# Kernel tuning notes

Measured on AMD Instinct MI355X. Metric: run time of the kernel, lower is better.

The kernel has to match this reference:

```python
import jax, jax.numpy as jnp
import numpy as np

LATENT = 128
HIDDEN = 512
N_STEPS = 50
BATCH = 8192


def _linear_init(k, fan_in, fan_out):
    kw, kb = jax.random.split(k)
    lim = 1.0 / np.sqrt(fan_in)
    W = jax.random.uniform(kw, (fan_in, fan_out), minval=-lim, maxval=lim, dtype=jnp.float32)
    b = jax.random.uniform(kb, (fan_out,), minval=-lim, maxval=lim, dtype=jnp.float32)
    return W, b


def setup_inputs() -> dict:
    key = jax.random.key(0)
    ks = jax.random.split(key, 6)
    in_dim = 2 * LATENT + 2  # x + condition + t_emb + target_emb
    W1, b1 = _linear_init(ks[0], in_dim, HIDDEN)
    W2, b2 = _linear_init(ks[1], HIDDEN, HIDDEN)
    W3, b3 = _linear_init(ks[2], HIDDEN, HIDDEN)
    W4, b4 = _linear_init(ks[3], HIDDEN, LATENT)
    condition = jax.random.normal(ks[4], (BATCH, LATENT), dtype=jnp.float32)
    x_init = jax.random.normal(ks[5], (BATCH, LATENT), dtype=jnp.float32)
    return dict(condition=condition, x_init=x_init,
                W1=W1, b1=b1, W2=W2, b2=b2, W3=W3, b3=b3, W4=W4, b4=b4,
                target_survival=1)


def reference(condition, x_init, W1, b1, W2, b2, W3, b3, W4, b4, target_survival):
    n_steps = N_STEPS
    betas = jnp.linspace(1e-4, 0.02, n_steps).astype(x_init.dtype)
    alphas = 1.0 - betas
    alphas_cumprod = jnp.cumprod(alphas)
    batch = condition.shape[0]
    # target = zeros if target_survival else ones (static python scalar)
    target = jnp.full((batch, 1), 0.0 if target_survival else 1.0, dtype=x_init.dtype)
    noise_key = jax.random.key(42)

    def step(x, t):
        t_emb = jnp.full((batch, 1), 1.0, x.dtype) * (t.astype(x.dtype) / n_steps)
        inp = jnp.concatenate([x, condition, t_emb, target], axis=-1)  # [B, 2L+2]
        h = jax.nn.gelu(inp @ W1 + b1, approximate=False)
        h = jax.nn.gelu(h @ W2 + b2, approximate=False)
        h = jax.nn.gelu(h @ W3 + b3, approximate=False)
        noise_pred = h @ W4 + b4  # [B, L]
        noise = jax.random.normal(jax.random.fold_in(noise_key, t), x.shape, x.dtype)
        noise = jnp.where(t > 0, noise, jnp.zeros_like(noise))  # no noise at t=0
        beta_t = betas[t]
        x = (x - beta_t / jnp.sqrt(1.0 - alphas_cumprod[t]) * noise_pred) / jnp.sqrt(alphas[t])
        x = x + jnp.sqrt(beta_t) * noise
        return x, None

    ts = jnp.arange(n_steps - 1, -1, -1)  # reversed(range(n_steps))
    x_final, _ = jax.lax.scan(step, x_init, ts)
    return x_final
```

## Files before the change

kernel.cpp:

```cpp
#include <hip/hip_runtime.h>
#include <stdint.h>
#include <stddef.h>


typedef __bf16 bf16;
typedef __bf16 bf16x4 __attribute__((ext_vector_type(4)));
typedef __bf16 bf16x8 __attribute__((ext_vector_type(8)));
typedef float  floatx4 __attribute__((ext_vector_type(4)));

#define NSTEPS    50
#define WG_ROWS   32
#define XB_STRIDE 136
#define H_STRIDE  520

__device__ __forceinline__ uint32_t rotl32(uint32_t x, int r) {
  return __builtin_amdgcn_alignbit(x, x, 32u - (uint32_t)r);
}

__device__ __forceinline__ void threefry2x32(uint32_t k0, uint32_t k1,
                                             uint32_t x0, uint32_t x1,
                                             uint32_t& o0, uint32_t& o1) {
  uint32_t k2 = k0 ^ k1 ^ 0x1BD11BDAu;
  x0 += k0; x1 += k1;
#define TF_R(R) { x0 += x1; x1 = rotl32(x1, R); x1 ^= x0; }
  TF_R(13) TF_R(15) TF_R(26) TF_R(6)
  x0 += k1; x1 += k2 + 1u;
  TF_R(17) TF_R(29) TF_R(16) TF_R(24)
  x0 += k2; x1 += k0 + 2u;
  TF_R(13) TF_R(15) TF_R(26) TF_R(6)
  x0 += k0; x1 += k1 + 3u;
  TF_R(17) TF_R(29) TF_R(16) TF_R(24)
  x0 += k1; x1 += k2 + 4u;
  TF_R(13) TF_R(15) TF_R(26) TF_R(6)
  x0 += k2; x1 += k0 + 5u;
#undef TF_R
  o0 = x0; o1 = x1;
}

__device__ __forceinline__ float erfinv_xla(float x) {
  float w = -0.6931471805599453f * __builtin_amdgcn_logf(fmaf(-x, x, 1.0f));
  float p;
  if (w < 5.0f) {
    w -= 2.5f;
    p = 2.81022636e-08f;
    p = fmaf(p, w, 3.43273939e-07f);
    p = fmaf(p, w, -3.5233877e-06f);
    p = fmaf(p, w, -4.39150654e-06f);
    p = fmaf(p, w, 0.00021858087f);
    p = fmaf(p, w, -0.00125372503f);
    p = fmaf(p, w, -0.00417768164f);
    p = fmaf(p, w, 0.246640727f);
    p = fmaf(p, w, 1.50140941f);
  } else {
    w = __builtin_amdgcn_sqrtf(w) - 3.0f;
    p = -0.000200214257f;
    p = fmaf(p, w, 0.000100950558f);
    p = fmaf(p, w, 0.00134934322f);
    p = fmaf(p, w, -0.00367342844f);
    p = fmaf(p, w, 0.00573950773f);
    p = fmaf(p, w, -0.0076224613f);
    p = fmaf(p, w, 0.00943887047f);
    p = fmaf(p, w, 1.00167406f);
    p = fmaf(p, w, 2.83297682f);
  }
  return p * x;
}

__device__ __forceinline__ float gelu_fast(float x) {
  float z  = x * 0.7071067811865475f;
  float az = fabsf(z);
  float t  = __builtin_amdgcn_rcpf(fmaf(0.3275911f, az, 1.0f));
  float p  = fmaf(1.061405429f, t, -1.453152027f);
  p = fmaf(p, t, 1.421413741f);
  p = fmaf(p, t, -0.284496736f);
  p = fmaf(p, t, 0.254829592f);
  p *= t;
  float e  = __builtin_amdgcn_exp2f(az * az * -1.4426950408889634f);
  float er = fmaf(-p, e, 1.0f);
  er = copysignf(er, z);
  return 0.5f * x * (1.0f + er);
}

template<int KSTEPS, int BSTRIDE, int UNROLL>
__device__ __forceinline__ void gemm2t(const bf16* __restrict__ h_lds,
                                       const bf16* __restrict__ A_pk,
                                       int lane, floatx4 (&acc)[2][2]) {
  const int nrow = lane & 15, q = lane >> 4;
  const bf16* b0 = h_lds + nrow * BSTRIDE + q * 8;
  const bf16* a0 = A_pk + lane * 8;
#pragma unroll UNROLL
  for (int ks = 0; ks < KSTEPS; ++ks) {
    bf16x8 bf0 = *(const bf16x8*)(b0 + ks * 32);
    bf16x8 bf1 = *(const bf16x8*)(b0 + 16 * BSTRIDE + ks * 32);
    bf16x8 aA  = *(const bf16x8*)(a0 + ks * 512);
    bf16x8 aB  = *(const bf16x8*)(a0 + (KSTEPS + ks) * 512);
    acc[0][0] = __builtin_amdgcn_mfma_f32_16x16x32_bf16(aA, bf0, acc[0][0], 0, 0, 0);
    acc[0][1] = __builtin_amdgcn_mfma_f32_16x16x32_bf16(aA, bf1, acc[0][1], 0, 0, 0);
    acc[1][0] = __builtin_amdgcn_mfma_f32_16x16x32_bf16(aB, bf0, acc[1][0], 0, 0, 0);
    acc[1][1] = __builtin_amdgcn_mfma_f32_16x16x32_bf16(aB, bf1, acc[1][1], 0, 0, 0);
  }
}

template<int KSTEPS, int BSTRIDE>
__device__ __forceinline__ void gemm1t(const bf16* __restrict__ h_lds,
                                       const bf16* __restrict__ A_pk,
                                       int lane, floatx4& acc) {
  const int nrow = lane & 15, q = lane >> 4;
  const bf16* b0 = h_lds + nrow * BSTRIDE + q * 8;
  const bf16* a0 = A_pk + lane * 8;
#pragma unroll 4
  for (int ks = 0; ks < KSTEPS; ++ks) {
    bf16x8 bfr = *(const bf16x8*)(b0 + ks * 32);
    bf16x8 af  = *(const bf16x8*)(a0 + ks * 512);
    acc = __builtin_amdgcn_mfma_f32_16x16x32_bf16(af, bfr, acc, 0, 0, 0);
  }
}

__global__ void diff_prep(const float* __restrict__ W1, const float* __restrict__ b1,
                          const float* __restrict__ W2, const float* __restrict__ W3,
                          const float* __restrict__ W4, const int* __restrict__ tsurv,
                          bf16* __restrict__ w1p, bf16* __restrict__ w1cp,
                          bf16* __restrict__ w2p, bf16* __restrict__ w3p,
                          bf16* __restrict__ w4p,
                          float* __restrict__ eb1, uint32_t* __restrict__ fk,
                          float* __restrict__ cst) {
  const int tid = blockIdx.x * blockDim.x + threadIdx.x;
  const int nth = gridDim.x * blockDim.x;
  for (int i = tid; i < 512 * 128; i += nth) {
    int j = i & 7, lane = (i >> 3) & 63, ks = (i >> 9) & 3, ntg = i >> 11;
    int n = ntg * 16 + (lane & 15);
    int k = ks * 32 + (lane >> 4) * 8 + j;
    w1p[i]  = (bf16)W1[k * 512 + n];
    w1cp[i] = (bf16)W1[(128 + k) * 512 + n];
  }
  for (int i = tid; i < 512 * 512; i += nth) {
    int j = i & 7, lane = (i >> 3) & 63, ks = (i >> 9) & 15, ntg = i >> 13;
    int n = ntg * 16 + (lane & 15);
    int k = ks * 32 + (lane >> 4) * 8 + j;
    w2p[i] = (bf16)W2[k * 512 + n];
    w3p[i] = (bf16)W3[k * 512 + n];
  }
  for (int i = tid; i < 128 * 512; i += nth) {
    int j = i & 7, lane = (i >> 3) & 63, ks = (i >> 9) & 15, ntg = i >> 13;
    int n = ntg * 16 + (lane & 15);
    int k = ks * 32 + (lane >> 4) * 8 + j;
    w4p[i] = (bf16)W4[k * 128 + n];
  }
  const float tgt = (tsurv[0] != 0) ? 0.0f : 1.0f;
  for (int i = tid; i < NSTEPS * 512; i += nth) {
    int t = i >> 9, n = i & 511;
    eb1[i] = b1[n] + ((float)t / 50.0f) * W1[256 * 512 + n] + tgt * W1[257 * 512 + n];
  }
  if (tid == 0) {
    float ac = 1.0f;
    for (int t = 0; t < NSTEPS; ++t) {
      float beta  = 1e-4f + (0.02f - 1e-4f) * ((float)t / 49.0f);
      float alpha = 1.0f - beta;
      ac *= alpha;
      cst[t]            = beta / sqrtf(1.0f - ac);
      cst[NSTEPS + t]   = 1.0f / sqrtf(alpha);
      cst[2*NSTEPS + t] = sqrtf(beta);
      uint32_t o0, o1;
      threefry2x32(0u, 42u, 0u, (uint32_t)t, o0, o1);
      fk[t] = o0; fk[NSTEPS + t] = o1;
    }
  }
}

__global__ __launch_bounds__(1024, 4) void diff_main(
    const float* __restrict__ cond, const float* __restrict__ xinit,
    const bf16* __restrict__ w1p, const bf16* __restrict__ w1cp,
    const bf16* __restrict__ w2p, const bf16* __restrict__ w3p,
    const bf16* __restrict__ w4p,
    const float* __restrict__ eb1, const float* __restrict__ b2,
    const float* __restrict__ b3, const float* __restrict__ b4,
    const uint32_t* __restrict__ fk, const float* __restrict__ cst,
    float* __restrict__ out) {
  __shared__ bf16 xb[WG_ROWS * XB_STRIDE];
  __shared__ bf16 hbA[WG_ROWS * H_STRIDE];
  __shared__ bf16 hbB[WG_ROWS * H_STRIDE];

  const int tid  = threadIdx.x;
  const int wave = tid >> 6;
  const int lane = tid & 63;
  const int nrow = lane & 15, q = lane >> 4;
  const int r0   = blockIdx.x * WG_ROWS;
  const int mc0  = wave * 32;
  const int qc   = q * 4;

  const int mtile4 = wave & 7;
  const int ntile4 = wave >> 3;
  const int n4     = ntile4 * 16 + nrow;
  const int xc0    = mtile4 * 16 + qc;

  {
    const int row = tid >> 5;
    const int c4  = (tid & 31) * 4;
    float4 a = *(const float4*)(xinit + (size_t)(r0 + row) * 128 + c4);
    float4 c = *(const float4*)(cond  + (size_t)(r0 + row) * 128 + c4);
    bf16x4 x4, c4v;
    x4[0] = (bf16)a.x; x4[1] = (bf16)a.y; x4[2] = (bf16)a.z; x4[3] = (bf16)a.w;
    c4v[0] = (bf16)c.x; c4v[1] = (bf16)c.y; c4v[2] = (bf16)c.z; c4v[3] = (bf16)c.w;
    *(bf16x4*)(xb  + row * XB_STRIDE + c4) = x4;
    *(bf16x4*)(hbA + row * H_STRIDE  + c4) = c4v;
  }
  float4 xreg = *(const float4*)(xinit + (size_t)(r0 + n4) * 128 + xc0);
  const uint32_t gbase = (uint32_t)(r0 + n4) * 128u + (uint32_t)xc0;
  __syncthreads();

  floatx4 cpr[2][2] = {};
  gemm2t<4, H_STRIDE, 4>(hbA, w1cp + (wave * 2) * 4 * 512, lane, cpr);
  __syncthreads();

  for (int t = NSTEPS - 1; t >= 0; --t) {
    float zn[4] = {0.0f, 0.0f, 0.0f, 0.0f};
    if (t > 0) {
      const uint32_t fk0 = fk[t], fk1 = fk[NSTEPS + t];
#pragma unroll
      for (int r = 0; r < 4; ++r) {
        uint32_t o0, o1;
        threefry2x32(fk0, fk1, 0u, gbase + (uint32_t)r, o0, o1);
        uint32_t bits = o0 ^ o1;
        float f01 = __uint_as_float((bits >> 9) | 0x3F800000u) - 1.0f;
        float u = f01 * 2.0f + (-0.99999994f);
        u = fmaxf(-0.99999994f, u);
        zn[r] = 1.4142135381698608f * erfinv_xla(u);
      }
    }

    {
      floatx4 acc[2][2] = {};
      gemm2t<4, XB_STRIDE, 4>(xb, w1p + (wave * 2) * 4 * 512, lane, acc);
      const float* ebt = eb1 + t * 512;
#pragma unroll
      for (int mt = 0; mt < 2; ++mt) {
        const int col = mc0 + mt * 16 + qc;
        float4 bb = *(const float4*)(ebt + col);
#pragma unroll
        for (int nt = 0; nt < 2; ++nt) {
          bf16x4 g;
#pragma unroll
          for (int r = 0; r < 4; ++r)
            g[r] = (bf16)gelu_fast(acc[mt][nt][r] + cpr[mt][nt][r] + ((const float*)&bb)[r]);
          *(bf16x4*)(hbA + (nt * 16 + nrow) * H_STRIDE + col) = g;
        }
      }
    }
    __syncthreads();

    {
      floatx4 acc[2][2] = {};
      gemm2t<16, H_STRIDE, 4>(hbA, w2p + (wave * 2) * 16 * 512, lane, acc);
#pragma unroll
      for (int mt = 0; mt < 2; ++mt) {
        const int col = mc0 + mt * 16 + qc;
        float4 bb = *(const float4*)(b2 + col);
#pragma unroll
        for (int nt = 0; nt < 2; ++nt) {
          bf16x4 g;
#pragma unroll
          for (int r = 0; r < 4; ++r)
            g[r] = (bf16)gelu_fast(acc[mt][nt][r] + ((const float*)&bb)[r]);
          *(bf16x4*)(hbB + (nt * 16 + nrow) * H_STRIDE + col) = g;
        }
      }
    }
    __syncthreads();

    {
      floatx4 acc[2][2] = {};
      gemm2t<16, H_STRIDE, 4>(hbB, w3p + (wave * 2) * 16 * 512, lane, acc);
#pragma unroll
      for (int mt = 0; mt < 2; ++mt) {
        const int col = mc0 + mt * 16 + qc;
        float4 bb = *(const float4*)(b3 + col);
#pragma unroll
        for (int nt = 0; nt < 2; ++nt) {
          bf16x4 g;
#pragma unroll
          for (int r = 0; r < 4; ++r)
            g[r] = (bf16)gelu_fast(acc[mt][nt][r] + ((const float*)&bb)[r]);
          *(bf16x4*)(hbA + (nt * 16 + nrow) * H_STRIDE + col) = g;
        }
      }
    }
    __syncthreads();

    {
      floatx4 acc = {};
      gemm1t<16, H_STRIDE>(hbA + ntile4 * 16 * H_STRIDE,
                           w4p + mtile4 * 16 * 512, lane, acc);
      const float c1 = cst[t], c2 = cst[NSTEPS + t], c3 = cst[2 * NSTEPS + t];
      float4 bb = *(const float4*)(b4 + xc0);
      bf16x4 xpk;
#pragma unroll
      for (int r = 0; r < 4; ++r) {
        float np = acc[r] + ((const float*)&bb)[r];
        float xn = (((float*)&xreg)[r] - c1 * np) * c2 + c3 * zn[r];
        ((float*)&xreg)[r] = xn;
        xpk[r] = (bf16)xn;
      }
      *(bf16x4*)(xb + n4 * XB_STRIDE + xc0) = xpk;
    }
    __syncthreads();
  }

  *(float4*)(out + (size_t)(r0 + n4) * 128 + xc0) = xreg;
}

extern "C" void kernel_launch(void* const* d_in, const int* in_sizes, int n_in,
                              void* d_out, int out_size, void* d_ws, size_t ws_size,
                              hipStream_t stream) {
  const float* cond  = (const float*)d_in[0];
  const float* xinit = (const float*)d_in[1];
  const float* W1 = (const float*)d_in[2];
  const float* b1 = (const float*)d_in[3];
  const float* W2 = (const float*)d_in[4];
  const float* b2 = (const float*)d_in[5];
  const float* W3 = (const float*)d_in[6];
  const float* b3 = (const float*)d_in[7];
  const float* W4 = (const float*)d_in[8];
  const float* b4 = (const float*)d_in[9];
  const int* tsurv = (const int*)d_in[10];

  char* ws = (char*)d_ws;
  bf16* w1p  = (bf16*)(ws + 0);
  bf16* w1cp = (bf16*)(ws + 131072);
  bf16* w2p  = (bf16*)(ws + 262144);
  bf16* w3p  = (bf16*)(ws + 786432);
  bf16* w4p  = (bf16*)(ws + 1310720);
  float* eb1 = (float*)(ws + 1441792);
  uint32_t* fkp = (uint32_t*)(ws + 1544192);
  float* cstp = (float*)(ws + 1544704);

  diff_prep<<<1024, 256, 0, stream>>>(W1, b1, W2, W3, W4, tsurv,
                                      w1p, w1cp, w2p, w3p, w4p, eb1, fkp, cstp);
  diff_main<<<256, 1024, 0, stream>>>(cond, xinit, w1p, w1cp, w2p, w3p, w4p,
                                      eb1, b2, b3, b4, fkp, cstp, (float*)d_out);
}
```

Before: 1.006 ms.

## Retile MLP GEMMs so each wave computes 64 columns for 16 rows

Changes the per-wave tiling of the fused MLP GEMMs. Before, each wave covered a 32x32 output tile (2 weight fragments x 2 activation fragments). Now it covers 64 output columns for a single 16-row half (4 weight fragments sharing one activation fragment). This halves LDS activation reads per wave but doubles the global/L2 weight fragment loads, since the pair of waves sharing a column slice both stream the same weights. The unroll factor is also reduced from 4 to 2. The layer-4 mapping is remapped to match.

```diff
diff --git a/kernel.cpp b/kernel.cpp
--- a/kernel.cpp
+++ b/kernel.cpp
@@ -82,22 +82,23 @@
 }
 
 template<int KSTEPS, int BSTRIDE, int UNROLL>
-__device__ __forceinline__ void gemm2t(const bf16* __restrict__ h_lds,
+__device__ __forceinline__ void gemm4t(const bf16* __restrict__ h_lds,
                                        const bf16* __restrict__ A_pk,
-                                       int lane, floatx4 (&acc)[2][2]) {
+                                       int lane, floatx4 (&acc)[4]) {
   const int nrow = lane & 15, q = lane >> 4;
   const bf16* b0 = h_lds + nrow * BSTRIDE + q * 8;
   const bf16* a0 = A_pk + lane * 8;
 #pragma unroll UNROLL
   for (int ks = 0; ks < KSTEPS; ++ks) {
-    bf16x8 bf0 = *(const bf16x8*)(b0 + ks * 32);
-    bf16x8 bf1 = *(const bf16x8*)(b0 + 16 * BSTRIDE + ks * 32);
-    bf16x8 aA  = *(const bf16x8*)(a0 + ks * 512);
-    bf16x8 aB  = *(const bf16x8*)(a0 + (KSTEPS + ks) * 512);
-    acc[0][0] = __builtin_amdgcn_mfma_f32_16x16x32_bf16(aA, bf0, acc[0][0], 0, 0, 0);
-    acc[0][1] = __builtin_amdgcn_mfma_f32_16x16x32_bf16(aA, bf1, acc[0][1], 0, 0, 0);
-    acc[1][0] = __builtin_amdgcn_mfma_f32_16x16x32_bf16(aB, bf0, acc[1][0], 0, 0, 0);
-    acc[1][1] = __builtin_amdgcn_mfma_f32_16x16x32_bf16(aB, bf1, acc[1][1], 0, 0, 0);
+    bf16x8 bfr = *(const bf16x8*)(b0 + ks * 32);
+    bf16x8 a0f = *(const bf16x8*)(a0 + (0 * KSTEPS + ks) * 512);
+    bf16x8 a1f = *(const bf16x8*)(a0 + (1 * KSTEPS + ks) * 512);
+    bf16x8 a2f = *(const bf16x8*)(a0 + (2 * KSTEPS + ks) * 512);
+    bf16x8 a3f = *(const bf16x8*)(a0 + (3 * KSTEPS + ks) * 512);
+    acc[0] = __builtin_amdgcn_mfma_f32_16x16x32_bf16(a0f, bfr, acc[0], 0, 0, 0);
+    acc[1] = __builtin_amdgcn_mfma_f32_16x16x32_bf16(a1f, bfr, acc[1], 0, 0, 0);
+    acc[2] = __builtin_amdgcn_mfma_f32_16x16x32_bf16(a2f, bfr, acc[2], 0, 0, 0);
+    acc[3] = __builtin_amdgcn_mfma_f32_16x16x32_bf16(a3f, bfr, acc[3], 0, 0, 0);
   }
 }
 
@@ -185,13 +186,13 @@
   const int lane = tid & 63;
   const int nrow = lane & 15, q = lane >> 4;
   const int r0   = blockIdx.x * WG_ROWS;
-  const int mc0  = wave * 32;
+  const int s    = wave >> 1;
+  const int g    = wave & 1;
+  const int mc0  = s * 64;
   const int qc   = q * 4;
 
-  const int mtile4 = wave & 7;
-  const int ntile4 = wave >> 3;
-  const int n4     = ntile4 * 16 + nrow;
-  const int xc0    = mtile4 * 16 + qc;
+  const int n4   = g * 16 + nrow;
+  const int xc0  = s * 16 + qc;
 
   {
     const int row = tid >> 5;
@@ -208,8 +209,8 @@
   const uint32_t gbase = (uint32_t)(r0 + n4) * 128u + (uint32_t)xc0;
   __syncthreads();
 
-  floatx4 cpr[2][2] = {};
-  gemm2t<4, H_STRIDE, 4>(hbA, w1cp + (wave * 2) * 4 * 512, lane, cpr);
+  floatx4 cpr[4] = {};
+  gemm4t<4, H_STRIDE, 2>(hbA + g * 16 * H_STRIDE, w1cp + s * 8192, lane, cpr);
   __syncthreads();
 
   for (int t = NSTEPS - 1; t >= 0; --t) {
@@ -229,67 +230,58 @@
     }
 
     {
-      floatx4 acc[2][2] = {};
-      gemm2t<4, XB_STRIDE, 4>(xb, w1p + (wave * 2) * 4 * 512, lane, acc);
+      floatx4 acc[4] = {};
+      gemm4t<4, XB_STRIDE, 2>(xb + g * 16 * XB_STRIDE, w1p + s * 8192, lane, acc);
       const float* ebt = eb1 + t * 512;
 #pragma unroll
-      for (int mt = 0; mt < 2; ++mt) {
+      for (int mt = 0; mt < 4; ++mt) {
         const int col = mc0 + mt * 16 + qc;
         float4 bb = *(const float4*)(ebt + col);
-#pragma unroll
-        for (int nt = 0; nt < 2; ++nt) {
-          bf16x4 g;
-#pragma unroll
-          for (int r = 0; r < 4; ++r)
-            g[r] = (bf16)gelu_fast(acc[mt][nt][r] + cpr[mt][nt][r] + ((const float*)&bb)[r]);
-          *(bf16x4*)(hbA + (nt * 16 + nrow) * H_STRIDE + col) = g;
-        }
+        bf16x4 gk;
+#pragma unroll
+        for (int r = 0; r < 4; ++r)
+          gk[r] = (bf16)gelu_fast(acc[mt][r] + cpr[mt][r] + ((const float*)&bb)[r]);
+        *(bf16x4*)(hbA + (g * 16 + nrow) * H_STRIDE + col) = gk;
       }
     }
     __syncthreads();
 
     {
-      floatx4 acc[2][2] = {};
-      gemm2t<16, H_STRIDE, 4>(hbA, w2p + (wave * 2) * 16 * 512, lane, acc);
-#pragma unroll
-      for (int mt = 0; mt < 2; ++mt) {
+      floatx4 acc[4] = {};
+      gemm4t<16, H_STRIDE, 2>(hbA + g * 16 * H_STRIDE, w2p + s * 32768, lane, acc);
+#pragma unroll
+      for (int mt = 0; mt < 4; ++mt) {
         const int col = mc0 + mt * 16 + qc;
         float4 bb = *(const float4*)(b2 + col);
-#pragma unroll
-        for (int nt = 0; nt < 2; ++nt) {
-          bf16x4 g;
-#pragma unroll
-          for (int r = 0; r < 4; ++r)
-            g[r] = (bf16)gelu_fast(acc[mt][nt][r] + ((const float*)&bb)[r]);
-          *(bf16x4*)(hbB + (nt * 16 + nrow) * H_STRIDE + col) = g;
-        }
+        bf16x4 gk;
+#pragma unroll
+        for (int r = 0; r < 4; ++r)
+          gk[r] = (bf16)gelu_fast(acc[mt][r] + ((const float*)&bb)[r]);
+        *(bf16x4*)(hbB + (g * 16 + nrow) * H_STRIDE + col) = gk;
       }
     }
     __syncthreads();
 
     {
-      floatx4 acc[2][2] = {};
-      gemm2t<16, H_STRIDE, 4>(hbB, w3p + (wave * 2) * 16 * 512, lane, acc);
-#pragma unroll
-      for (int mt = 0; mt < 2; ++mt) {
+      floatx4 acc[4] = {};
+      gemm4t<16, H_STRIDE, 2>(hbB + g * 16 * H_STRIDE, w3p + s * 32768, lane, acc);
+#pragma unroll
+      for (int mt = 0; mt < 4; ++mt) {
         const int col = mc0 + mt * 16 + qc;
         float4 bb = *(const float4*)(b3 + col);
-#pragma unroll
-        for (int nt = 0; nt < 2; ++nt) {
-          bf16x4 g;
-#pragma unroll
-          for (int r = 0; r < 4; ++r)
-            g[r] = (bf16)gelu_fast(acc[mt][nt][r] + ((const float*)&bb)[r]);
-          *(bf16x4*)(hbA + (nt * 16 + nrow) * H_STRIDE + col) = g;
-        }
+        bf16x4 gk;
+#pragma unroll
+        for (int r = 0; r < 4; ++r)
+          gk[r] = (bf16)gelu_fast(acc[mt][r] + ((const float*)&bb)[r]);
+        *(bf16x4*)(hbA + (g * 16 + nrow) * H_STRIDE + col) = gk;
       }
     }
     __syncthreads();
 
     {
       floatx4 acc = {};
-      gemm1t<16, H_STRIDE>(hbA + ntile4 * 16 * H_STRIDE,
-                           w4p + mtile4 * 16 * 512, lane, acc);
+      gemm1t<16, H_STRIDE>(hbA + g * 16 * H_STRIDE,
+                           w4p + s * 16 * 512, lane, acc);
       const float c1 = cst[t], c2 = cst[NSTEPS + t], c3 = cst[2 * NSTEPS + t];
       float4 bb = *(const float4*)(b4 + xc0);
       bf16x4 xpk;
```

New measurement: 1.372 ms. 36.3% more time.
